# Kernel tuning notes

Measured on AMD Instinct MI355X. Metric: run time of the kernel, lower is better.

Reference implementation:

```python
import jax, jax.numpy as jnp
import numpy as np


def gcn_conv(x, W, b, src, dst, n):
    """PyG GCNConv: D^-1/2 (A+I) D^-1/2 X W + b, with added self-loops."""
    xw = x @ W  # [N, out]
    loop = jnp.arange(n, dtype=src.dtype)
    s = jnp.concatenate([src, loop])
    d = jnp.concatenate([dst, loop])
    deg = jax.ops.segment_sum(jnp.ones_like(d, dtype=xw.dtype), d, num_segments=n)
    dinv = jax.lax.rsqrt(jnp.maximum(deg, 1.0))
    norm = dinv[s] * dinv[d]  # [E+N]
    msg = xw[s] * norm[:, None]  # [E+N, out]
    return jax.ops.segment_sum(msg, d, num_segments=n) + b


def mean_pool(h, batch, num_graphs):
    s = jax.ops.segment_sum(h, batch, num_segments=num_graphs)
    cnt = jax.ops.segment_sum(jnp.ones((h.shape[0],), h.dtype), batch, num_segments=num_graphs)
    return s / jnp.maximum(cnt, 1.0)[:, None]


def setup_inputs() -> dict:
    key = jax.random.key(0)
    ks = jax.random.split(key, 12)
    N, E, F_dim, H_dim, K = 50000, 1600000, 128, 128, 32
    G = 64
    X = jax.random.normal(ks[0], (N, F_dim), dtype=jnp.float32)
    ei_feat = jax.random.randint(ks[1], (2, E), 0, N, dtype=jnp.int64)
    batch = jnp.sort(jax.random.randint(ks[2], (N,), 0, G, dtype=jnp.int64))
    sc = 1.0 / np.sqrt(H_dim)
    W1 = jax.random.normal(ks[3], (F_dim, H_dim), dtype=jnp.float32) * sc
    b1 = jnp.zeros((H_dim,), jnp.float32)
    W2 = jax.random.normal(ks[4], (H_dim, K), dtype=jnp.float32) * sc
    b2 = jnp.zeros((K,), jnp.float32)
    mW1 = jax.random.normal(ks[5], (H_dim, H_dim), dtype=jnp.float32) * sc
    mb1 = jnp.zeros((H_dim,), jnp.float32)
    mW2 = jax.random.normal(ks[6], (K, K), dtype=jnp.float32) * (1.0 / np.sqrt(K))
    mb2 = jnp.zeros((K,), jnp.float32)
    return {"X": X, "W1": W1, "b1": b1, "W2": W2, "b2": b2,
            "mW1": mW1, "mb1": mb1, "mW2": mW2, "mb2": mb2,
            "ei_feat": ei_feat, "batch": batch, "num_graphs": G}


def reference(X, W1, b1, W2, b2, mW1, mb1, mW2, mb2, ei_feat, batch, num_graphs):
    N = X.shape[0]
    src, dst = ei_feat[0], ei_feat[1]
    h = jax.nn.elu(gcn_conv(X, W1, b1, src, dst, N))  # [N, H]
    master_h = mean_pool(h, batch, num_graphs)  # [G, H]
    h = h + jax.nn.relu(master_h @ mW1 + mb1)[batch]
    Z = gcn_conv(h, W2, b2, src, dst, N)  # [N, K]
    master_z = mean_pool(Z, batch, num_graphs)  # [G, K]
    Z = Z + jax.nn.relu(master_z @ mW2 + mb2)[batch]
    return jax.nn.softmax(Z, axis=1)
```

## Files before the change

### kernel.cpp

```cpp
#include <hip/hip_runtime.h>
#include <hip/hip_bf16.h>
#include <hip/hip_fp16.h>

#define DEV_INLINE __device__ __forceinline__

static DEV_INLINE float4 ld4(const float* p){ return *reinterpret_cast<const float4*>(p); }

#define GNUM 64
#define CHUNK 4096
#define MAXNB 1024
#define CAP 8192

typedef _Float16 half8 __attribute__((ext_vector_type(8)));
typedef float floatx4 __attribute__((ext_vector_type(4)));

#define W1T_ELEMS (128*136)
#define W2T_ELEMS (32*136)

__global__ __launch_bounds__(256) void k_scatter(const int* __restrict__ src, const int* __restrict__ dst,
                                                 int E, int NB, int* __restrict__ bfill,
                                                 unsigned* __restrict__ ebuf,
                                                 const float* __restrict__ W1, const float* __restrict__ W2,
                                                 __half* __restrict__ w1t, __half* __restrict__ w2t, int EB){
    if ((int)blockIdx.x >= EB){
        int f = ((int)blockIdx.x - EB)*256 + threadIdx.x;
        if (f < W1T_ELEMS){
            int c = f/136, k = f - c*136;
            w1t[f] = (k<128) ? __float2half(W1[k*128+c]) : __float2half(0.f);
        } else {
            int f2 = f - W1T_ELEMS;
            if (f2 < W2T_ELEMS){
                int c = f2/136, k = f2 - c*136;
                w2t[f2] = (k<128) ? __float2half(W2[k*32+c]) : __float2half(0.f);
            }
        }
        return;
    }
    __shared__ int cnt[MAXNB];
    __shared__ int pfx[MAXNB];
    __shared__ int gbase[MAXNB];
    __shared__ unsigned stage[CHUNK];
    __shared__ int ws[4];
    int t = threadIdx.x; int base0 = blockIdx.x*CHUNK;
    int tot = E - base0; if (tot > CHUNK) tot = CHUNK;
    for (int i=t;i<NB;i+=256) cnt[i]=0;
    __syncthreads();
    unsigned v[16]; int rk[16];
    #pragma unroll
    for (int k=0;k<16;k++){
        int o = t + k*256;
        if (o < tot){
            int e = base0 + o;
            int s = src[e], d = dst[e];
            v[k] = (unsigned)s | ((unsigned)d<<16);
            rk[k] = atomicAdd(&cnt[d>>7], 1);
        } else { v[k]=0u; rk[k]=-1; }
    }
    __syncthreads();
    int i0 = t*4;
    int c0=(i0+0<NB)?cnt[i0+0]:0, c1=(i0+1<NB)?cnt[i0+1]:0;
    int c2=(i0+2<NB)?cnt[i0+2]:0, c3=(i0+3<NB)?cnt[i0+3]:0;
    int tsum=c0+c1+c2+c3;
    int lane=t&63, w=t>>6;
    int x=tsum;
    for (int off=1;off<64;off<<=1){ int yv=__shfl_up(x,off); if (lane>=off) x+=yv; }
    if (lane==63) ws[w]=x;
    __syncthreads();
    if (t==0){ int a=0; for (int i=0;i<4;i++){ int tmp=ws[i]; ws[i]=a; a+=tmp; } }
    __syncthreads();
    int ex = x - tsum + ws[w];
    if (i0+0<NB) pfx[i0+0]=ex; ex+=c0;
    if (i0+1<NB) pfx[i0+1]=ex; ex+=c1;
    if (i0+2<NB) pfx[i0+2]=ex; ex+=c2;
    if (i0+3<NB) pfx[i0+3]=ex;
    __syncthreads();
    for (int i=t;i<NB;i+=256){
        int c = cnt[i];
        if (c){
            int base = atomicAdd(&bfill[i], c);
            if (base > CAP - c) base = CAP - c;
            gbase[i] = i*CAP + base;
        } else gbase[i] = 0;
    }
    __syncthreads();
    #pragma unroll
    for (int k=0;k<16;k++) if (rk[k]>=0){ int b = (int)(v[k]>>23); stage[pfx[b]+rk[k]] = v[k]; }
    __syncthreads();
    for (int j=t;j<tot;j+=256){
        unsigned u = stage[j];
        int b = (int)(u>>23);
        ebuf[gbase[b] + (j - pfx[b])] = u;
    }
}

__global__ __launch_bounds__(256) void k_bucket_finish(const unsigned* __restrict__ ebuf,
                                                       const int* __restrict__ bfill,
                                                       int2* __restrict__ rs2, unsigned short* __restrict__ csr,
                                                       float* __restrict__ dinv,
                                                       const int* __restrict__ batch, int* __restrict__ gstart,
                                                       int N){
    __shared__ int c2[128];
    __shared__ int rsl[128];
    __shared__ int ws[4];
    int b = blockIdx.x, t = threadIdx.x;
    if (b == 0 && t >= 128 && t < 128 + GNUM + 1){
        int g = t - 128;
        int lo = 0, hi = N;
        while (lo < hi){ int mid = (lo+hi)>>1; if (batch[mid] < g) lo = mid+1; else hi = mid; }
        gstart[g] = lo;
    }
    if (t < 128) c2[t] = 0;
    __syncthreads();
    int s0 = b*CAP;
    int cntB = bfill[b]; if (cntB > CAP) cntB = CAP;
    int s1 = s0 + cntB;
    for (int j = s0+t; j < s1; j += 256)
        atomicAdd(&c2[(ebuf[j]>>16)&127], 1);
    __syncthreads();
    int v = (t < 128) ? c2[t] : 0;
    int lane = t & 63, w = t >> 6;
    int x = v;
    for (int off=1; off<64; off<<=1){
        int yv = __shfl_up(x, off);
        if (lane >= off) x += yv;
    }
    if (lane == 63) ws[w] = x;
    __syncthreads();
    if (t < 128){
        int ex = x - v + ((w == 1) ? ws[0] : 0);
        rsl[t] = s0 + ex;
        int node = (b<<7) + t;
        if (node < N){
            rs2[node] = make_int2(s0 + ex, s0 + ex + v);
            dinv[node] = rsqrtf((float)(v + 1));
        }
    }
    __syncthreads();
    if (t < 128) c2[t] = 0;
    __syncthreads();
    for (int j = s0+t; j < s1; j += 256){
        unsigned u = ebuf[j];
        int ld = (u>>16)&127;
        int p = atomicAdd(&c2[ld], 1);
        csr[rsl[ld]+p] = (unsigned short)(u & 0xffffu);
    }
}

__global__ __launch_bounds__(256) void k_gemm1(const float* __restrict__ X, const __half* __restrict__ w1t,
                                               const float* __restrict__ dinv, __half* __restrict__ yh, int N){
    __shared__ __half Wl[128*136];
    int t = threadIdx.x;
    if (blockIdx.x==0 && t < 32)
        reinterpret_cast<uint2*>(yh + (size_t)N*128)[t] = make_uint2(0u,0u);
    {
        const uint4* g = (const uint4*)w1t;
        uint4* l = (uint4*)Wl;
        for (int i = t; i < 2176; i += 256) l[i] = g[i];
    }
    __syncthreads();
    int wv = t>>6, lane = t&63;
    int r0 = blockIdx.x*64 + wv*16;
    if (r0 >= N) return;
    int lr = lane & 15, lg = lane >> 4;
    int r = r0 + lr;
    bool rok = r < N;
    const float* xrow = X + (size_t)(rok ? r : 0)*128;
    floatx4 acc[8];
    #pragma unroll
    for (int i=0;i<8;i++) acc[i] = (floatx4){0.f,0.f,0.f,0.f};
    #pragma unroll
    for (int ks=0; ks<4; ks++){
        int k0 = ks*32 + lg*8;
        float4 xa = ld4(xrow + k0);
        float4 xb = ld4(xrow + k0 + 4);
        half8 bfrag;
        bfrag[0]=(_Float16)xa.x; bfrag[1]=(_Float16)xa.y; bfrag[2]=(_Float16)xa.z; bfrag[3]=(_Float16)xa.w;
        bfrag[4]=(_Float16)xb.x; bfrag[5]=(_Float16)xb.y; bfrag[6]=(_Float16)xb.z; bfrag[7]=(_Float16)xb.w;
        #pragma unroll
        for (int ct=0; ct<8; ct++){
            half8 afrag = *reinterpret_cast<const half8*>(&Wl[(ct*16 + lr)*136 + k0]);
            acc[ct] = __builtin_amdgcn_mfma_f32_16x16x32_f16(afrag, bfrag, acc[ct], 0, 0, 0);
        }
    }
    if (rok){
        float dv = dinv[r];
        #pragma unroll
        for (int ct=0; ct<8; ct++){
            __half2 p0 = __floats2half2_rn(acc[ct][0]*dv, acc[ct][1]*dv);
            __half2 p1 = __floats2half2_rn(acc[ct][2]*dv, acc[ct][3]*dv);
            uint2 stv; stv.x = *(unsigned*)&p0; stv.y = *(unsigned*)&p1;
            *reinterpret_cast<uint2*>(&yh[(size_t)r*128 + ct*16 + lg*4]) = stv;
        }
    }
}

__global__ void k_agg1(const __half* __restrict__ yh, const float* __restrict__ dinv,
                       const float* __restrict__ b1, const int2* __restrict__ rs2,
                       const unsigned short* __restrict__ csr, __half* __restrict__ h, int N){
    int wid = (int)((blockIdx.x * blockDim.x + threadIdx.x) >> 6);
    if (wid >= N) return;
    int lane = threadIdx.x & 63;
    int q = lane >> 4, ql = lane & 15;
    int2 se = rs2[wid];
    int beg = se.x, end = se.y;
    int len = end - beg;
    int qlen = (len + 3) >> 2;
    int qbeg = beg + q*qlen;
    int qend = qbeg + qlen; if (qend > end) qend = end;
    int mylen = qend - qbeg; if (mylen < 0) mylen = 0;
    const char* yb = (const char*)yh;
    unsigned lofs = (unsigned)ql * 16u;
    float f0=0.f,f1=0.f,f2=0.f,f3=0.f,f4=0.f,f5=0.f,f6=0.f,f7=0.f;
    int iters = (qlen + 15) >> 4;
    for (int c=0;c<iters;c++){
        int o = c*16 + ql;
        int idx = (o < mylen) ? (int)csr[qbeg + o] : N;
        int tmax = qlen - c*16; if (tmax > 16) tmax = 16;
        int nch = (tmax + 7) >> 3;
        __half2 a0 = __float2half2_rn(0.f), a1 = a0, a2 = a0, a3 = a0;
        for (int ch=0; ch<nch; ++ch){
            int tb = (q<<4) + ch*8;
            int s0 = __shfl(idx, tb+0);
            int s1 = __shfl(idx, tb+1);
            int s2 = __shfl(idx, tb+2);
            int s3 = __shfl(idx, tb+3);
            int s4 = __shfl(idx, tb+4);
            int s5 = __shfl(idx, tb+5);
            int s6 = __shfl(idx, tb+6);
            int s7 = __shfl(idx, tb+7);
            uint4 u0 = *(const uint4*)(yb + (((unsigned)s0<<8) + lofs));
            uint4 u1 = *(const uint4*)(yb + (((unsigned)s1<<8) + lofs));
            uint4 u2 = *(const uint4*)(yb + (((unsigned)s2<<8) + lofs));
            uint4 u3 = *(const uint4*)(yb + (((unsigned)s3<<8) + lofs));
            uint4 u4 = *(const uint4*)(yb + (((unsigned)s4<<8) + lofs));
            uint4 u5 = *(const uint4*)(yb + (((unsigned)s5<<8) + lofs));
            uint4 u6 = *(const uint4*)(yb + (((unsigned)s6<<8) + lofs));
            uint4 u7 = *(const uint4*)(yb + (((unsigned)s7<<8) + lofs));
            a0 = __hadd2(a0, *(__half2*)&u0.x); a1 = __hadd2(a1, *(__half2*)&u0.y);
            a2 = __hadd2(a2, *(__half2*)&u0.z); a3 = __hadd2(a3, *(__half2*)&u0.w);
            a0 = __hadd2(a0, *(__half2*)&u1.x); a1 = __hadd2(a1, *(__half2*)&u1.y);
            a2 = __hadd2(a2, *(__half2*)&u1.z); a3 = __hadd2(a3, *(__half2*)&u1.w);
            a0 = __hadd2(a0, *(__half2*)&u2.x); a1 = __hadd2(a1, *(__half2*)&u2.y);
            a2 = __hadd2(a2, *(__half2*)&u2.z); a3 = __hadd2(a3, *(__half2*)&u2.w);
            a0 = __hadd2(a0, *(__half2*)&u3.x); a1 = __hadd2(a1, *(__half2*)&u3.y);
            a2 = __hadd2(a2, *(__half2*)&u3.z); a3 = __hadd2(a3, *(__half2*)&u3.w);
            a0 = __hadd2(a0, *(__half2*)&u4.x); a1 = __hadd2(a1, *(__half2*)&u4.y);
            a2 = __hadd2(a2, *(__half2*)&u4.z); a3 = __hadd2(a3, *(__half2*)&u4.w);
            a0 = __hadd2(a0, *(__half2*)&u5.x); a1 = __hadd2(a1, *(__half2*)&u5.y);
            a2 = __hadd2(a2, *(__half2*)&u5.z); a3 = __hadd2(a3, *(__half2*)&u5.w);
            a0 = __hadd2(a0, *(__half2*)&u6.x); a1 = __hadd2(a1, *(__half2*)&u6.y);
            a2 = __hadd2(a2, *(__half2*)&u6.z); a3 = __hadd2(a3, *(__half2*)&u6.w);
            a0 = __hadd2(a0, *(__half2*)&u7.x); a1 = __hadd2(a1, *(__half2*)&u7.y);
            a2 = __hadd2(a2, *(__half2*)&u7.z); a3 = __hadd2(a3, *(__half2*)&u7.w);
        }
        float2 t0 = __half22float2(a0); f0 += t0.x; f1 += t0.y;
        float2 t1 = __half22float2(a1); f2 += t1.x; f3 += t1.y;
        float2 t2 = __half22float2(a2); f4 += t2.x; f5 += t2.y;
        float2 t3 = __half22float2(a3); f6 += t3.x; f7 += t3.y;
    }
    f0 += __shfl_xor(f0,16); f1 += __shfl_xor(f1,16); f2 += __shfl_xor(f2,16); f3 += __shfl_xor(f3,16);
    f4 += __shfl_xor(f4,16); f5 += __shfl_xor(f5,16); f6 += __shfl_xor(f6,16); f7 += __shfl_xor(f7,16);
    f0 += __shfl_xor(f0,32); f1 += __shfl_xor(f1,32); f2 += __shfl_xor(f2,32); f3 += __shfl_xor(f3,32);
    f4 += __shfl_xor(f4,32); f5 += __shfl_xor(f5,32); f6 += __shfl_xor(f6,32); f7 += __shfl_xor(f7,32);
    if (q == 0){
        uint4 su = *(const uint4*)(yb + (((unsigned)wid<<8) + lofs));
        float2 s0 = __half22float2(*(__half2*)&su.x); f0 += s0.x; f1 += s0.y;
        float2 s1 = __half22float2(*(__half2*)&su.y); f2 += s1.x; f3 += s1.y;
        float2 s2 = __half22float2(*(__half2*)&su.z); f4 += s2.x; f5 += s2.y;
        float2 s3 = __half22float2(*(__half2*)&su.w); f6 += s3.x; f7 += s3.y;
        float dv = dinv[wid];
        float4 ba = ld4(&b1[ql*8]), bb = ld4(&b1[ql*8+4]);
        float o0 = dv*f0+ba.x, o1 = dv*f1+ba.y, o2 = dv*f2+ba.z, o3 = dv*f3+ba.w;
        float o4 = dv*f4+bb.x, o5 = dv*f5+bb.y, o6 = dv*f6+bb.z, o7 = dv*f7+bb.w;
        o0 = o0>0.f?o0:expm1f(o0); o1 = o1>0.f?o1:expm1f(o1);
        o2 = o2>0.f?o2:expm1f(o2); o3 = o3>0.f?o3:expm1f(o3);
        o4 = o4>0.f?o4:expm1f(o4); o5 = o5>0.f?o5:expm1f(o5);
        o6 = o6>0.f?o6:expm1f(o6); o7 = o7>0.f?o7:expm1f(o7);
        __half2 p0 = __floats2half2_rn(o0,o1), p1 = __floats2half2_rn(o2,o3);
        __half2 p2 = __floats2half2_rn(o4,o5), p3 = __floats2half2_rn(o6,o7);
        uint4 stv; stv.x=*(unsigned*)&p0; stv.y=*(unsigned*)&p1; stv.z=*(unsigned*)&p2; stv.w=*(unsigned*)&p3;
        *reinterpret_cast<uint4*>(&h[(size_t)wid*128 + ql*8]) = stv;
    }
}

__global__ void k_mpoolh(const __half* __restrict__ hsrc, const int* __restrict__ gstart,
                         float* __restrict__ msum){
    int g = blockIdx.x, part = blockIdx.y, P = gridDim.y;
    int c = threadIdx.x;
    int s0 = gstart[g], s1 = gstart[g+1];
    int len = s1 - s0;
    int per = (len + P - 1) / P;
    int rbeg = s0 + part*per, rend = rbeg + per; if (rend > s1) rend = s1;
    float sx = 0.f, sy = 0.f;
    const __half2* h2 = (const __half2*)hsrc;
    for (int r = rbeg; r < rend; ++r){
        float2 f = __half22float2(h2[(size_t)r*64 + c]);
        sx += f.x; sy += f.y;
    }
    if (rend > rbeg){
        atomicAdd(&msum[g*128 + 2*c], sx);
        atomicAdd(&msum[g*128 + 2*c+1], sy);
    }
}

__global__ void k_mpool(const float* __restrict__ srcm, const int* __restrict__ gstart,
                        float* __restrict__ msum, int C){
    int g = blockIdx.x, part = blockIdx.y, P = gridDim.y;
    int c = threadIdx.x;
    if (c >= C) return;
    int s0 = gstart[g], s1 = gstart[g+1];
    int len = s1 - s0;
    int per = (len + P - 1) / P;
    int rbeg = s0 + part*per, rend = rbeg + per; if (rend > s1) rend = s1;
    float sum = 0.f;
    for (int r = rbeg; r < rend; ++r) sum += srcm[(size_t)r*C + c];
    if (rend > rbeg) atomicAdd(&msum[g*C + c], sum);
}

__global__ void k_mlp1(const float* __restrict__ msum, const int* __restrict__ gstart,
                       const float* __restrict__ mW1, const float* __restrict__ mb1,
                       __half* __restrict__ r1h){
    int g = blockIdx.x, c = threadIdx.x;
    int cnt = gstart[g+1] - gstart[g];
    float inv = 1.f / (float)(cnt > 1 ? cnt : 1);
    float acc = mb1[c];
    for (int k=0;k<128;k++) acc = fmaf(msum[g*128+k]*inv, mW1[k*128+c], acc);
    r1h[g*128+c] = __float2half(fmaxf(acc, 0.f));
}

__global__ void k_mlp2(const float* __restrict__ msum2, const int* __restrict__ gstart,
                       const float* __restrict__ mW2, const float* __restrict__ mb2,
                       float* __restrict__ r2){
    int g = blockIdx.x, c = threadIdx.x;
    if (c >= 32) return;
    int cnt = gstart[g+1] - gstart[g];
    float inv = 1.f / (float)(cnt > 1 ? cnt : 1);
    float acc = mb2[c];
    for (int k=0;k<32;k++) acc = fmaf(msum2[g*32+k]*inv, mW2[k*32+c], acc);
    r2[g*32+c] = fmaxf(acc, 0.f);
}

__global__ __launch_bounds__(256) void k_gemm2(const __half* __restrict__ h, const __half* __restrict__ r1h,
                                               const int* __restrict__ batch, const __half* __restrict__ w2t,
                                               const float* __restrict__ dinv, __half* __restrict__ y2, int N){
    __shared__ __half Wl[32*136];
    int t = threadIdx.x;
    if (blockIdx.x==0 && t < 8)
        reinterpret_cast<uint2*>(y2 + (size_t)N*32)[t] = make_uint2(0u,0u);
    {
        const uint4* g = (const uint4*)w2t;
        uint4* l = (uint4*)Wl;
        for (int i = t; i < 544; i += 256) l[i] = g[i];
    }
    __syncthreads();
    int wv = t>>6, lane = t&63;
    int r0 = blockIdx.x*64 + wv*16;
    if (r0 >= N) return;
    int lr = lane & 15, lg = lane >> 4;
    int r = r0 + lr;
    bool rok = r < N;
    int rr = rok ? r : 0;
    const __half* hrow = h + (size_t)rr*128;
    const __half* vrow = r1h + (size_t)batch[rr]*128;
    floatx4 acc0 = (floatx4){0.f,0.f,0.f,0.f};
    floatx4 acc1 = (floatx4){0.f,0.f,0.f,0.f};
    #pragma unroll
    for (int ks=0; ks<4; ks++){
        int k0 = ks*32 + lg*8;
        uint4 hu = *reinterpret_cast<const uint4*>(hrow + k0);
        uint4 vu = *reinterpret_cast<const uint4*>(vrow + k0);
        __half2 b0 = __hadd2(*(__half2*)&hu.x, *(__half2*)&vu.x);
        __half2 b1_ = __hadd2(*(__half2*)&hu.y, *(__half2*)&vu.y);
        __half2 b2_ = __hadd2(*(__half2*)&hu.z, *(__half2*)&vu.z);
        __half2 b3_ = __hadd2(*(__half2*)&hu.w, *(__half2*)&vu.w);
        uint4 bu; bu.x=*(unsigned*)&b0; bu.y=*(unsigned*)&b1_; bu.z=*(unsigned*)&b2_; bu.w=*(unsigned*)&b3_;
        half8 bfrag = *reinterpret_cast<half8*>(&bu);
        half8 a0 = *reinterpret_cast<const half8*>(&Wl[(0*16 + lr)*136 + k0]);
        half8 a1 = *reinterpret_cast<const half8*>(&Wl[(1*16 + lr)*136 + k0]);
        acc0 = __builtin_amdgcn_mfma_f32_16x16x32_f16(a0, bfrag, acc0, 0, 0, 0);
        acc1 = __builtin_amdgcn_mfma_f32_16x16x32_f16(a1, bfrag, acc1, 0, 0, 0);
    }
    if (rok){
        float dv = dinv[r];
        {
            __half2 p0 = __floats2half2_rn(acc0[0]*dv, acc0[1]*dv);
            __half2 p1 = __floats2half2_rn(acc0[2]*dv, acc0[3]*dv);
            uint2 stv; stv.x = *(unsigned*)&p0; stv.y = *(unsigned*)&p1;
            *reinterpret_cast<uint2*>(&y2[(size_t)r*32 + 0 + lg*4]) = stv;
        }
        {
            __half2 p0 = __floats2half2_rn(acc1[0]*dv, acc1[1]*dv);
            __half2 p1 = __floats2half2_rn(acc1[2]*dv, acc1[3]*dv);
            uint2 stv; stv.x = *(unsigned*)&p0; stv.y = *(unsigned*)&p1;
            *reinterpret_cast<uint2*>(&y2[(size_t)r*32 + 16 + lg*4]) = stv;
        }
    }
}

__global__ void k_agg2h(const __half* __restrict__ y2, const float* __restrict__ dinv,
                        const float* __restrict__ b2, const int2* __restrict__ rs2,
                        const unsigned short* __restrict__ csr, float* __restrict__ Z, int N){
    int wid = (int)((blockIdx.x*blockDim.x + threadIdx.x) >> 6);
    if (wid >= N) return;
    int lane = threadIdx.x & 63;
    int o8 = lane >> 3, ol = lane & 7;
    int2 se = rs2[wid];
    int beg = se.x, end = se.y, len = end-beg;
    int olen = (len + 7) >> 3;
    int obeg = beg + o8*olen;
    int oend = obeg + olen; if (oend > end) oend = end;
    int mylen = oend - obeg; if (mylen < 0) mylen = 0;
    const char* yb = (const char*)y2;
    unsigned lofs = (unsigned)ol * 8u;
    float f0=0.f, f1=0.f, f2=0.f, f3=0.f;
    int iters = (olen + 7) >> 3;
    for (int c=0;c<iters;c++){
        int o = c*8 + ol;
        int idx = (o < mylen) ? (int)csr[obeg + o] : N;
        int tb = o8<<3;
        int s0 = __shfl(idx, tb+0);
        int s1 = __shfl(idx, tb+1);
        int s2 = __shfl(idx, tb+2);
        int s3 = __shfl(idx, tb+3);
        int s4 = __shfl(idx, tb+4);
        int s5 = __shfl(idx, tb+5);
        int s6 = __shfl(idx, tb+6);
        int s7 = __shfl(idx, tb+7);
        uint2 u0 = *(const uint2*)(yb + (((unsigned)s0<<6) + lofs));
        uint2 u1 = *(const uint2*)(yb + (((unsigned)s1<<6) + lofs));
        uint2 u2 = *(const uint2*)(yb + (((unsigned)s2<<6) + lofs));
        uint2 u3 = *(const uint2*)(yb + (((unsigned)s3<<6) + lofs));
        uint2 u4 = *(const uint2*)(yb + (((unsigned)s4<<6) + lofs));
        uint2 u5 = *(const uint2*)(yb + (((unsigned)s5<<6) + lofs));
        uint2 u6 = *(const uint2*)(yb + (((unsigned)s6<<6) + lofs));
        uint2 u7 = *(const uint2*)(yb + (((unsigned)s7<<6) + lofs));
        __half2 a0 = __float2half2_rn(0.f), a1 = a0;
        a0 = __hadd2(a0, *(__half2*)&u0.x); a1 = __hadd2(a1, *(__half2*)&u0.y);
        a0 = __hadd2(a0, *(__half2*)&u1.x); a1 = __hadd2(a1, *(__half2*)&u1.y);
        a0 = __hadd2(a0, *(__half2*)&u2.x); a1 = __hadd2(a1, *(__half2*)&u2.y);
        a0 = __hadd2(a0, *(__half2*)&u3.x); a1 = __hadd2(a1, *(__half2*)&u3.y);
        a0 = __hadd2(a0, *(__half2*)&u4.x); a1 = __hadd2(a1, *(__half2*)&u4.y);
        a0 = __hadd2(a0, *(__half2*)&u5.x); a1 = __hadd2(a1, *(__half2*)&u5.y);
        a0 = __hadd2(a0, *(__half2*)&u6.x); a1 = __hadd2(a1, *(__half2*)&u6.y);
        a0 = __hadd2(a0, *(__half2*)&u7.x); a1 = __hadd2(a1, *(__half2*)&u7.y);
        float2 t0 = __half22float2(a0); f0 += t0.x; f1 += t0.y;
        float2 t1 = __half22float2(a1); f2 += t1.x; f3 += t1.y;
    }
    f0 += __shfl_xor(f0,8);  f1 += __shfl_xor(f1,8);  f2 += __shfl_xor(f2,8);  f3 += __shfl_xor(f3,8);
    f0 += __shfl_xor(f0,16); f1 += __shfl_xor(f1,16); f2 += __shfl_xor(f2,16); f3 += __shfl_xor(f3,16);
    f0 += __shfl_xor(f0,32); f1 += __shfl_xor(f1,32); f2 += __shfl_xor(f2,32); f3 += __shfl_xor(f3,32);
    if (o8 == 0){
        uint2 su = *(const uint2*)(yb + (((unsigned)wid<<6) + lofs));
        float2 s0 = __half22float2(*(__half2*)&su.x); f0 += s0.x; f1 += s0.y;
        float2 s1 = __half22float2(*(__half2*)&su.y); f2 += s1.x; f3 += s1.y;
        float dv = dinv[wid];
        float4 bb = ld4(&b2[ol*4]);
        float4 outv;
        outv.x = dv*f0 + bb.x; outv.y = dv*f1 + bb.y;
        outv.z = dv*f2 + bb.z; outv.w = dv*f3 + bb.w;
        *reinterpret_cast<float4*>(&Z[(size_t)wid*32 + ol*4]) = outv;
    }
}

__global__ void k_softmax(float* __restrict__ Z, const float* __restrict__ r2,
                          const int* __restrict__ batch, int N){
    int r = blockIdx.x*8 + (threadIdx.x>>5);
    int c = threadIdx.x & 31;
    if (r >= N) return;
    float z = Z[(size_t)r*32+c] + r2[batch[r]*32 + c];
    float m = z;
    #pragma unroll
    for (int off=16; off>=1; off>>=1) m = fmaxf(m, __shfl_xor(m, off));
    float e = expf(z - m);
    float s = e;
    #pragma unroll
    for (int off=16; off>=1; off>>=1) s += __shfl_xor(s, off);
    Z[(size_t)r*32+c] = e / s;
}

extern "C" void kernel_launch(void* const* d_in, const int* in_sizes, int n_in,
                              void* d_out, int out_size, void* d_ws, size_t ws_size,
                              hipStream_t stream){
    const float* X   = (const float*)d_in[0];
    const float* W1  = (const float*)d_in[1];
    const float* b1  = (const float*)d_in[2];
    const float* W2  = (const float*)d_in[3];
    const float* b2  = (const float*)d_in[4];
    const float* mW1 = (const float*)d_in[5];
    const float* mb1 = (const float*)d_in[6];
    const float* mW2 = (const float*)d_in[7];
    const float* mb2 = (const float*)d_in[8];
    const int*   ei  = (const int*)d_in[9];
    const int*   batch = (const int*)d_in[10];
    int N = in_sizes[0] / 128;
    int E = in_sizes[9] / 2;
    const int* src = ei;
    const int* dst = ei + E;
    float* Zout = (float*)d_out;

    char* wsp = (char*)d_ws;
    size_t off = 0;
    auto alloc = [&](size_t bytes)->char*{
        char* p = wsp + off; off += (bytes + 255) & ~(size_t)255; return p;
    };
    int*   bfill = (int*)  alloc((size_t)MAXNB*4);
    float* msum  = (float*)alloc((size_t)GNUM*128*4);
    float* msum2 = (float*)alloc((size_t)GNUM*32*4);
    size_t zero_bytes = off;
    int NB = (N + 127) >> 7;
    int2*  rs2   = (int2*) alloc((size_t)N*8);
    int*   gstart= (int*)  alloc((GNUM+1)*4);
    unsigned* ebuf = (unsigned*)alloc((size_t)NB*CAP*4);
    unsigned short* csr = (unsigned short*)alloc((size_t)NB*CAP*2);
    float* dinvp = (float*)alloc((size_t)N*4);
    __half* w1t  = (__half*)alloc((size_t)W1T_ELEMS*2);
    __half* w2t  = (__half*)alloc((size_t)W2T_ELEMS*2);
    __half* yh   = (__half*)alloc((size_t)(N+1)*128*2);
    __half* h    = (__half*)alloc((size_t)N*128*2);
    __half* y2h  = (__half*)alloc((size_t)(N+1)*32*2);
    __half* r1buf= (__half*)alloc((size_t)GNUM*128*2);
    float* r2buf = (float*)alloc((size_t)GNUM*32*4);
    (void)ws_size; (void)n_in; (void)out_size;

    hipMemsetAsync(d_ws, 0, zero_bytes, stream);

    int EB = (E + CHUNK-1) / CHUNK;
    int PREP = (W1T_ELEMS + W2T_ELEMS + 255)/256;

    k_scatter      <<<EB + PREP, 256, 0, stream>>>(src, dst, E, NB, bfill, ebuf, W1, W2, w1t, w2t, EB);
    k_bucket_finish<<<NB, 256, 0, stream>>>(ebuf, bfill, rs2, csr, dinvp, batch, gstart, N);

    k_gemm1 <<<(N+63)/64, 256, 0, stream>>>(X, w1t, dinvp, yh, N);
    k_agg1  <<<(N+3)/4, 256, 0, stream>>>(yh, dinvp, b1, rs2, csr, h, N);

    k_mpoolh<<<dim3(GNUM,8), 64, 0, stream>>>(h, gstart, msum);
    k_mlp1  <<<GNUM, 128, 0, stream>>>(msum, gstart, mW1, mb1, r1buf);

    k_gemm2 <<<(N+63)/64, 256, 0, stream>>>(h, r1buf, batch, w2t, dinvp, y2h, N);
    k_agg2h <<<(N+3)/4, 256, 0, stream>>>(y2h, dinvp, b2, rs2, csr, Zout, N);

    k_mpool <<<dim3(GNUM,8), 64, 0, stream>>>(Zout, gstart, msum2, 32);
    k_mlp2  <<<GNUM, 64, 0, stream>>>(msum2, gstart, mW2, mb2, r2buf);
    k_softmax<<<(N+7)/8, 256, 0, stream>>>(Zout, r2buf, batch, N);
}
```

Baseline: 210.6 us.

## Sort CSR neighbors by source tile, interleave lanes, fuse pooling with MLP

The CSR build now sorts each node's neighbor list by which quarter of the node range the source falls in. The aggregation kernels hand out neighbors to lane groups in an interleaved way, so at any step all groups gather from the same region of the feature table, which should improve L2 locality. The mean-pool and virtual-node MLP kernels are merged into one block per graph. That removes the atomics, the memset'd sum buffers and two launches, but leaves only 64 blocks to run the pooling reductions.

```diff
diff --git a/kernel.cpp b/kernel.cpp
--- a/kernel.cpp
+++ b/kernel.cpp
@@ -16,6 +16,14 @@
 
 #define W1T_ELEMS (128*136)
 #define W2T_ELEMS (32*136)
+
+static DEV_INLINE int tile_of(int s, int TS){
+    int t = 0;
+    if (s >= TS)   t = 1;
+    if (s >= 2*TS) t = 2;
+    if (s >= 3*TS) t = 3;
+    return t;
+}
 
 __global__ __launch_bounds__(256) void k_scatter(const int* __restrict__ src, const int* __restrict__ dst,
                                                  int E, int NB, int* __restrict__ bfill,
@@ -98,51 +106,63 @@
                                                        int2* __restrict__ rs2, unsigned short* __restrict__ csr,
                                                        float* __restrict__ dinv,
                                                        const int* __restrict__ batch, int* __restrict__ gstart,
-                                                       int N){
-    __shared__ int c2[128];
-    __shared__ int rsl[128];
+                                                       int N, int TS){
+    __shared__ int c2[512];
+    __shared__ int rsl[512];
     __shared__ int ws[4];
     int b = blockIdx.x, t = threadIdx.x;
+    for (int i=t;i<512;i+=256) c2[i]=0;
     if (b == 0 && t >= 128 && t < 128 + GNUM + 1){
         int g = t - 128;
         int lo = 0, hi = N;
         while (lo < hi){ int mid = (lo+hi)>>1; if (batch[mid] < g) lo = mid+1; else hi = mid; }
         gstart[g] = lo;
     }
-    if (t < 128) c2[t] = 0;
     __syncthreads();
     int s0 = b*CAP;
     int cntB = bfill[b]; if (cntB > CAP) cntB = CAP;
     int s1 = s0 + cntB;
-    for (int j = s0+t; j < s1; j += 256)
-        atomicAdd(&c2[(ebuf[j]>>16)&127], 1);
-    __syncthreads();
-    int v = (t < 128) ? c2[t] : 0;
+    for (int j = s0+t; j < s1; j += 256){
+        unsigned u = ebuf[j];
+        int key = (((u>>16)&127)<<2) | tile_of((int)(u & 0xffffu), TS);
+        atomicAdd(&c2[key], 1);
+    }
+    __syncthreads();
+    int i0 = t*2;
+    int v0 = c2[i0], v1 = c2[i0+1];
+    int tsum = v0 + v1;
     int lane = t & 63, w = t >> 6;
-    int x = v;
+    int x = tsum;
     for (int off=1; off<64; off<<=1){
         int yv = __shfl_up(x, off);
         if (lane >= off) x += yv;
     }
     if (lane == 63) ws[w] = x;
     __syncthreads();
+    if (t == 0){ int a=0; for (int i=0;i<4;i++){ int tmp=ws[i]; ws[i]=a; a+=tmp; } }
+    __syncthreads();
+    int ex = x - tsum + ws[w];
+    rsl[i0]   = s0 + ex;
+    rsl[i0+1] = s0 + ex + v0;
+    __syncthreads();
     if (t < 128){
-        int ex = x - v + ((w == 1) ? ws[0] : 0);
-        rsl[t] = s0 + ex;
+        int start = rsl[t<<2];
+        int end   = (t < 127) ? rsl[(t+1)<<2] : s1;
         int node = (b<<7) + t;
         if (node < N){
-            rs2[node] = make_int2(s0 + ex, s0 + ex + v);
-            dinv[node] = rsqrtf((float)(v + 1));
-        }
-    }
-    __syncthreads();
-    if (t < 128) c2[t] = 0;
+            rs2[node] = make_int2(start, end);
+            dinv[node] = rsqrtf((float)(end - start + 1));
+        }
+    }
+    __syncthreads();
+    for (int i=t;i<512;i+=256) c2[i]=0;
     __syncthreads();
     for (int j = s0+t; j < s1; j += 256){
         unsigned u = ebuf[j];
-        int ld = (u>>16)&127;
-        int p = atomicAdd(&c2[ld], 1);
-        csr[rsl[ld]+p] = (unsigned short)(u & 0xffffu);
+        int s = (int)(u & 0xffffu);
+        int key = (((u>>16)&127)<<2) | tile_of(s, TS);
+        int p = atomicAdd(&c2[key], 1);
+        csr[rsl[key]+p] = (unsigned short)s;
     }
 }
 
@@ -205,16 +225,14 @@
     int beg = se.x, end = se.y;
     int len = end - beg;
     int qlen = (len + 3) >> 2;
-    int qbeg = beg + q*qlen;
-    int qend = qbeg + qlen; if (qend > end) qend = end;
-    int mylen = qend - qbeg; if (mylen < 0) mylen = 0;
     const char* yb = (const char*)yh;
     unsigned lofs = (unsigned)ql * 16u;
     float f0=0.f,f1=0.f,f2=0.f,f3=0.f,f4=0.f,f5=0.f,f6=0.f,f7=0.f;
     int iters = (qlen + 15) >> 4;
     for (int c=0;c<iters;c++){
         int o = c*16 + ql;
-        int idx = (o < mylen) ? (int)csr[qbeg + o] : N;
+        int j = (o<<2) + q;
+        int idx = (j < len) ? (int)csr[beg + j] : N;
         int tmax = qlen - c*16; if (tmax > 16) tmax = 16;
         int nch = (tmax + 7) >> 3;
         __half2 a0 = __float2half2_rn(0.f), a1 = a0, a2 = a0, a3 = a0;
@@ -283,61 +301,60 @@
     }
 }
 
-__global__ void k_mpoolh(const __half* __restrict__ hsrc, const int* __restrict__ gstart,
-                         float* __restrict__ msum){
-    int g = blockIdx.x, part = blockIdx.y, P = gridDim.y;
-    int c = threadIdx.x;
+__global__ __launch_bounds__(256) void k_vn1(const __half* __restrict__ h, const int* __restrict__ gstart,
+                                             const float* __restrict__ mW1, const float* __restrict__ mb1,
+                                             __half* __restrict__ r1h){
+    __shared__ float sums[4][128];
+    __shared__ float msum[128];
+    int g = blockIdx.x, t = threadIdx.x;
     int s0 = gstart[g], s1 = gstart[g+1];
-    int len = s1 - s0;
-    int per = (len + P - 1) / P;
-    int rbeg = s0 + part*per, rend = rbeg + per; if (rend > s1) rend = s1;
+    int c2i = t & 63, rg = t >> 6;
+    const __half2* h2 = (const __half2*)h;
     float sx = 0.f, sy = 0.f;
-    const __half2* h2 = (const __half2*)hsrc;
-    for (int r = rbeg; r < rend; ++r){
-        float2 f = __half22float2(h2[(size_t)r*64 + c]);
+    for (int r = s0+rg; r < s1; r += 4){
+        float2 f = __half22float2(h2[(size_t)r*64 + c2i]);
         sx += f.x; sy += f.y;
     }
-    if (rend > rbeg){
-        atomicAdd(&msum[g*128 + 2*c], sx);
-        atomicAdd(&msum[g*128 + 2*c+1], sy);
-    }
-}
-
-__global__ void k_mpool(const float* __restrict__ srcm, const int* __restrict__ gstart,
-                        float* __restrict__ msum, int C){
-    int g = blockIdx.x, part = blockIdx.y, P = gridDim.y;
-    int c = threadIdx.x;
-    if (c >= C) return;
+    sums[rg][2*c2i] = sx; sums[rg][2*c2i+1] = sy;
+    __syncthreads();
+    if (t < 128){
+        float s = sums[0][t]+sums[1][t]+sums[2][t]+sums[3][t];
+        int cnt = s1 - s0;
+        msum[t] = s / (float)(cnt > 1 ? cnt : 1);
+    }
+    __syncthreads();
+    if (t < 128){
+        float acc = mb1[t];
+        for (int k=0;k<128;k++) acc = fmaf(msum[k], mW1[k*128+t], acc);
+        r1h[g*128+t] = __float2half(fmaxf(acc, 0.f));
+    }
+}
+
+__global__ __launch_bounds__(256) void k_vn2(const float* __restrict__ Z, const int* __restrict__ gstart,
+                                             const float* __restrict__ mW2, const float* __restrict__ mb2,
+                                             float* __restrict__ r2){
+    __shared__ float sums[8][32];
+    __shared__ float msum[32];
+    int g = blockIdx.x, t = threadIdx.x;
     int s0 = gstart[g], s1 = gstart[g+1];
-    int len = s1 - s0;
-    int per = (len + P - 1) / P;
-    int rbeg = s0 + part*per, rend = rbeg + per; if (rend > s1) rend = s1;
-    float sum = 0.f;
-    for (int r = rbeg; r < rend; ++r) sum += srcm[(size_t)r*C + c];
-    if (rend > rbeg) atomicAdd(&msum[g*C + c], sum);
-}
-
-__global__ void k_mlp1(const float* __restrict__ msum, const int* __restrict__ gstart,
-                       const float* __restrict__ mW1, const float* __restrict__ mb1,
-                       __half* __restrict__ r1h){
-    int g = blockIdx.x, c = threadIdx.x;
-    int cnt = gstart[g+1] - gstart[g];
-    float inv = 1.f / (float)(cnt > 1 ? cnt : 1);
-    float acc = mb1[c];
-    for (int k=0;k<128;k++) acc = fmaf(msum[g*128+k]*inv, mW1[k*128+c], acc);
-    r1h[g*128+c] = __float2half(fmaxf(acc, 0.f));
-}
-
-__global__ void k_mlp2(const float* __restrict__ msum2, const int* __restrict__ gstart,
-                       const float* __restrict__ mW2, const float* __restrict__ mb2,
-                       float* __restrict__ r2){
-    int g = blockIdx.x, c = threadIdx.x;
-    if (c >= 32) return;
-    int cnt = gstart[g+1] - gstart[g];
-    float inv = 1.f / (float)(cnt > 1 ? cnt : 1);
-    float acc = mb2[c];
-    for (int k=0;k<32;k++) acc = fmaf(msum2[g*32+k]*inv, mW2[k*32+c], acc);
-    r2[g*32+c] = fmaxf(acc, 0.f);
+    int col = t & 31, rg = t >> 5;
+    float s = 0.f;
+    for (int r = s0+rg; r < s1; r += 8) s += Z[(size_t)r*32 + col];
+    sums[rg][col] = s;
+    __syncthreads();
+    if (t < 32){
+        float v = 0.f;
+        #pragma unroll
+        for (int i=0;i<8;i++) v += sums[i][t];
+        int cnt = s1 - s0;
+        msum[t] = v / (float)(cnt > 1 ? cnt : 1);
+    }
+    __syncthreads();
+    if (t < 32){
+        float acc = mb2[t];
+        for (int k=0;k<32;k++) acc = fmaf(msum[k], mW2[k*32+t], acc);
+        r2[g*32+t] = fmaxf(acc, 0.f);
+    }
 }
 
 __global__ __launch_bounds__(256) void k_gemm2(const __half* __restrict__ h, const __half* __restrict__ r1h,
@@ -407,16 +424,14 @@
     int2 se = rs2[wid];
     int beg = se.x, end = se.y, len = end-beg;
     int olen = (len + 7) >> 3;
-    int obeg = beg + o8*olen;
-    int oend = obeg + olen; if (oend > end) oend = end;
-    int mylen = oend - obeg; if (mylen < 0) mylen = 0;
     const char* yb = (const char*)y2;
     unsigned lofs = (unsigned)ol * 8u;
     float f0=0.f, f1=0.f, f2=0.f, f3=0.f;
     int iters = (olen + 7) >> 3;
     for (int c=0;c<iters;c++){
         int o = c*8 + ol;
-        int idx = (o < mylen) ? (int)csr[obeg + o] : N;
+        int j = (o<<3) + o8;
+        int idx = (j < len) ? (int)csr[beg + j] : N;
         int tb = o8<<3;
         int s0 = __shfl(idx, tb+0);
         int s1 = __shfl(idx, tb+1);
@@ -504,8 +519,6 @@
         char* p = wsp + off; off += (bytes + 255) & ~(size_t)255; return p;
     };
     int*   bfill = (int*)  alloc((size_t)MAXNB*4);
-    float* msum  = (float*)alloc((size_t)GNUM*128*4);
-    float* msum2 = (float*)alloc((size_t)GNUM*32*4);
     size_t zero_bytes = off;
     int NB = (N + 127) >> 7;
     int2*  rs2   = (int2*) alloc((size_t)N*8);
@@ -526,20 +539,19 @@
 
     int EB = (E + CHUNK-1) / CHUNK;
     int PREP = (W1T_ELEMS + W2T_ELEMS + 255)/256;
+    int TS = (N + 3)/4;
 
     k_scatter      <<<EB + PREP, 256, 0, stream>>>(src, dst, E, NB, bfill, ebuf, W1, W2, w1t, w2t, EB);
-    k_bucket_finish<<<NB, 256, 0, stream>>>(ebuf, bfill, rs2, csr, dinvp, batch, gstart, N);
+    k_bucket_finish<<<NB, 256, 0, stream>>>(ebuf, bfill, rs2, csr, dinvp, batch, gstart, N, TS);
 
     k_gemm1 <<<(N+63)/64, 256, 0, stream>>>(X, w1t, dinvp, yh, N);
     k_agg1  <<<(N+3)/4, 256, 0, stream>>>(yh, dinvp, b1, rs2, csr, h, N);
 
-    k_mpoolh<<<dim3(GNUM,8), 64, 0, stream>>>(h, gstart, msum);
-    k_mlp1  <<<GNUM, 128, 0, stream>>>(msum, gstart, mW1, mb1, r1buf);
+    k_vn1   <<<GNUM, 256, 0, stream>>>(h, gstart, mW1, mb1, r1buf);
 
     k_gemm2 <<<(N+63)/64, 256, 0, stream>>>(h, r1buf, batch, w2t, dinvp, y2h, N);
     k_agg2h <<<(N+3)/4, 256, 0, stream>>>(y2h, dinvp, b2, rs2, csr, Zout, N);
 
-    k_mpool <<<dim3(GNUM,8), 64, 0, stream>>>(Zout, gstart, msum2, 32);
-    k_mlp2  <<<GNUM, 64, 0, stream>>>(msum2, gstart, mW2, mb2, r2buf);
+    k_vn2   <<<GNUM, 256, 0, stream>>>(Zout, gstart, mW2, mb2, r2buf);
     k_softmax<<<(N+7)/8, 256, 0, stream>>>(Zout, r2buf, batch, N);
 }
```

Result: slower. 230.2 us (+9.3%).

## Sort CSR neighbors by source-node tile and interleave lane assignment in aggregation

Applied to the files above, without the earlier changes.

The CSR build now sub-buckets each destination's neighbor list by which quarter of the node range the source falls in, using 512 shared counters and a full-block scan. The aggregation kernels switch from contiguous per-quarter/octet segments to a strided interleave, so lanes fetching in the same step touch sources from the same node-range tile. The aim is better L2/cache locality for the gathered feature rows. In exchange the bucket kernel does extra compare work and a wider scan, and the interleave has to stay consistent with the per-group loop bounds.

```diff
diff --git a/kernel.cpp b/kernel.cpp
--- a/kernel.cpp
+++ b/kernel.cpp
@@ -16,6 +16,14 @@
 
 #define W1T_ELEMS (128*136)
 #define W2T_ELEMS (32*136)
+
+static DEV_INLINE int tile_of(int s, int TS){
+    int t = 0;
+    if (s >= TS)   t = 1;
+    if (s >= 2*TS) t = 2;
+    if (s >= 3*TS) t = 3;
+    return t;
+}
 
 __global__ __launch_bounds__(256) void k_scatter(const int* __restrict__ src, const int* __restrict__ dst,
                                                  int E, int NB, int* __restrict__ bfill,
@@ -98,51 +106,63 @@
                                                        int2* __restrict__ rs2, unsigned short* __restrict__ csr,
                                                        float* __restrict__ dinv,
                                                        const int* __restrict__ batch, int* __restrict__ gstart,
-                                                       int N){
-    __shared__ int c2[128];
-    __shared__ int rsl[128];
+                                                       int N, int TS){
+    __shared__ int c2[512];
+    __shared__ int rsl[512];
     __shared__ int ws[4];
     int b = blockIdx.x, t = threadIdx.x;
+    for (int i=t;i<512;i+=256) c2[i]=0;
     if (b == 0 && t >= 128 && t < 128 + GNUM + 1){
         int g = t - 128;
         int lo = 0, hi = N;
         while (lo < hi){ int mid = (lo+hi)>>1; if (batch[mid] < g) lo = mid+1; else hi = mid; }
         gstart[g] = lo;
     }
-    if (t < 128) c2[t] = 0;
     __syncthreads();
     int s0 = b*CAP;
     int cntB = bfill[b]; if (cntB > CAP) cntB = CAP;
     int s1 = s0 + cntB;
-    for (int j = s0+t; j < s1; j += 256)
-        atomicAdd(&c2[(ebuf[j]>>16)&127], 1);
-    __syncthreads();
-    int v = (t < 128) ? c2[t] : 0;
+    for (int j = s0+t; j < s1; j += 256){
+        unsigned u = ebuf[j];
+        int key = (((u>>16)&127)<<2) | tile_of((int)(u & 0xffffu), TS);
+        atomicAdd(&c2[key], 1);
+    }
+    __syncthreads();
+    int i0 = t*2;
+    int v0 = c2[i0], v1 = c2[i0+1];
+    int tsum = v0 + v1;
     int lane = t & 63, w = t >> 6;
-    int x = v;
+    int x = tsum;
     for (int off=1; off<64; off<<=1){
         int yv = __shfl_up(x, off);
         if (lane >= off) x += yv;
     }
     if (lane == 63) ws[w] = x;
     __syncthreads();
+    if (t == 0){ int a=0; for (int i=0;i<4;i++){ int tmp=ws[i]; ws[i]=a; a+=tmp; } }
+    __syncthreads();
+    int ex = x - tsum + ws[w];
+    rsl[i0]   = s0 + ex;
+    rsl[i0+1] = s0 + ex + v0;
+    __syncthreads();
     if (t < 128){
-        int ex = x - v + ((w == 1) ? ws[0] : 0);
-        rsl[t] = s0 + ex;
+        int start = rsl[t<<2];
+        int end   = (t < 127) ? rsl[(t+1)<<2] : s1;
         int node = (b<<7) + t;
         if (node < N){
-            rs2[node] = make_int2(s0 + ex, s0 + ex + v);
-            dinv[node] = rsqrtf((float)(v + 1));
-        }
-    }
-    __syncthreads();
-    if (t < 128) c2[t] = 0;
+            rs2[node] = make_int2(start, end);
+            dinv[node] = rsqrtf((float)(end - start + 1));
+        }
+    }
+    __syncthreads();
+    for (int i=t;i<512;i+=256) c2[i]=0;
     __syncthreads();
     for (int j = s0+t; j < s1; j += 256){
         unsigned u = ebuf[j];
-        int ld = (u>>16)&127;
-        int p = atomicAdd(&c2[ld], 1);
-        csr[rsl[ld]+p] = (unsigned short)(u & 0xffffu);
+        int s = (int)(u & 0xffffu);
+        int key = (((u>>16)&127)<<2) | tile_of(s, TS);
+        int p = atomicAdd(&c2[key], 1);
+        csr[rsl[key]+p] = (unsigned short)s;
     }
 }
 
@@ -205,16 +225,14 @@
     int beg = se.x, end = se.y;
     int len = end - beg;
     int qlen = (len + 3) >> 2;
-    int qbeg = beg + q*qlen;
-    int qend = qbeg + qlen; if (qend > end) qend = end;
-    int mylen = qend - qbeg; if (mylen < 0) mylen = 0;
     const char* yb = (const char*)yh;
     unsigned lofs = (unsigned)ql * 16u;
     float f0=0.f,f1=0.f,f2=0.f,f3=0.f,f4=0.f,f5=0.f,f6=0.f,f7=0.f;
     int iters = (qlen + 15) >> 4;
     for (int c=0;c<iters;c++){
         int o = c*16 + ql;
-        int idx = (o < mylen) ? (int)csr[qbeg + o] : N;
+        int j = (o<<2) + q;
+        int idx = (j < len) ? (int)csr[beg + j] : N;
         int tmax = qlen - c*16; if (tmax > 16) tmax = 16;
         int nch = (tmax + 7) >> 3;
         __half2 a0 = __float2half2_rn(0.f), a1 = a0, a2 = a0, a3 = a0;
@@ -407,16 +425,14 @@
     int2 se = rs2[wid];
     int beg = se.x, end = se.y, len = end-beg;
     int olen = (len + 7) >> 3;
-    int obeg = beg + o8*olen;
-    int oend = obeg + olen; if (oend > end) oend = end;
-    int mylen = oend - obeg; if (mylen < 0) mylen = 0;
     const char* yb = (const char*)y2;
     unsigned lofs = (unsigned)ol * 8u;
     float f0=0.f, f1=0.f, f2=0.f, f3=0.f;
     int iters = (olen + 7) >> 3;
     for (int c=0;c<iters;c++){
         int o = c*8 + ol;
-        int idx = (o < mylen) ? (int)csr[obeg + o] : N;
+        int j = (o<<3) + o8;
+        int idx = (j < len) ? (int)csr[beg + j] : N;
         int tb = o8<<3;
         int s0 = __shfl(idx, tb+0);
         int s1 = __shfl(idx, tb+1);
@@ -526,9 +542,10 @@
 
     int EB = (E + CHUNK-1) / CHUNK;
     int PREP = (W1T_ELEMS + W2T_ELEMS + 255)/256;
+    int TS = (N + 3)/4;
 
     k_scatter      <<<EB + PREP, 256, 0, stream>>>(src, dst, E, NB, bfill, ebuf, W1, W2, w1t, w2t, EB);
-    k_bucket_finish<<<NB, 256, 0, stream>>>(ebuf, bfill, rs2, csr, dinvp, batch, gstart, N);
+    k_bucket_finish<<<NB, 256, 0, stream>>>(ebuf, bfill, rs2, csr, dinvp, batch, gstart, N, TS);
 
     k_gemm1 <<<(N+63)/64, 256, 0, stream>>>(X, w1t, dinvp, yh, N);
     k_agg1  <<<(N+3)/4, 256, 0, stream>>>(yh, dinvp, b1, rs2, csr, h, N);
```

After: 213.0 us. About the same (+1.1%).
